# Kernel optimization log

Hardware: AMD Instinct MI355X
Metric: run time of the kernel (lower is better)

Reference implementation:

```python
import jax, jax.numpy as jnp
import numpy as np

DIM, NUM_HEADS, N_POINTS = 256, 8, 4
N_Q, N_KV = 32768, 32768


def setup_inputs() -> dict:
    key = jax.random.key(0)
    ks = jax.random.split(key, 16)
    C, H, P = DIM, NUM_HEADS, N_POINTS
    s = 1.0 / np.sqrt(C)
    inp = {
        "query": jax.random.normal(ks[0], (N_Q, C), jnp.float32),
        "key": jax.random.normal(ks[1], (N_KV, C), jnp.float32),
        "value": jax.random.normal(ks[2], (N_KV, C), jnp.float32),
        # reference_points: Linear(C, 2*H*P)
        "Wr": jax.random.normal(ks[3], (C, 2 * H * P), jnp.float32) * s,
        "br": jnp.zeros((2 * H * P,), jnp.float32),
        # offset_attn: Linear(C, H*P*2)
        "Wo": jax.random.normal(ks[4], (C, H * P * 2), jnp.float32) * s,
        "bo": jnp.zeros((H * P * 2,), jnp.float32),
        # value_proj: Linear(C, C)
        "Wv": jax.random.normal(ks[5], (C, C), jnp.float32) * s,
        "bv": jnp.zeros((C,), jnp.float32),
        # output_proj: Linear(C, C)
        "Wout": jax.random.normal(ks[6], (C, C), jnp.float32) * s,
        "bout": jnp.zeros((C,), jnp.float32),
    }
    return inp


def reference(query, key, value, Wr, br, Wo, bo, Wv, bv, Wout, bout):
    N, C = query.shape
    M = value.shape[0]
    H, P = NUM_HEADS, N_POINTS
    Ch = C // H

    # sampling locations in [0,1] (ref) plus unconstrained offsets
    ref = jax.nn.sigmoid((query @ Wr + br).reshape(N, H, P, 2))
    off = (query @ Wo + bo).reshape(N, H, P, 2)
    loc = ref + off                              # [N,H,P,2]

    # 1-D bilinear interpolation along the token axis. The original's
    # 4-term (wx,wy) expression algebraically collapses to a pure lerp in x:
    # (1-wx)(1-wy)+ (1-wx)wy = (1-wx), wx(1-wy)+wx*wy = wx.
    x = loc[..., 0] * (M - 1)                    # [N,H,P]
    x0 = jnp.clip(jnp.floor(x).astype(jnp.int32), 0, M - 1)
    x1 = jnp.clip(x0 + 1, 0, M - 1)
    wx = (x - x0.astype(x.dtype))[..., None]     # [N,H,P,1]

    hidx = jnp.arange(H)[None, :, None]          # head-aligned gather index

    def sample(table):                           # table: [M,H,Ch]
        g0 = table[x0, hidx]                     # [N,H,P,Ch]
        g1 = table[x1, hidx]
        return (1.0 - wx) * g0 + wx * g1

    v = (value @ Wv + bv).reshape(M, H, Ch)      # value_proj, split heads
    sv = sample(v)                               # [N,H,P,Ch] sampled values

    # attention weights from query/key: sample per-head keys at the same
    # locations, dot with per-head queries, softmax over the P points
    k = key.reshape(M, H, Ch)
    sk = sample(k)                               # [N,H,P,Ch]
    q = query.reshape(N, H, Ch)
    scores = jnp.einsum("nhc,nhpc->nhp", q, sk) / jnp.sqrt(
        jnp.asarray(Ch, query.dtype)
    )
    attn = jax.nn.softmax(scores, axis=-1)       # [N,H,P]

    out = jnp.einsum("nhp,nhpc->nhc", attn, sv).reshape(N, C)
    return out @ Wout + bout
```

## Files before the change

kernel.cpp:

```cpp
#include <hip/hip_runtime.h>
#include <hip/hip_bf16.h>
#include <stdint.h>

#define NQ    32768
#define NKV   32768
#define CDIM  256
#define NHEADS 8
#define NPTS  4

using bf16x8 = __attribute__((ext_vector_type(8))) short;
using f32x4  = __attribute__((ext_vector_type(4))) float;
using u16x8  = __attribute__((ext_vector_type(8))) ushort;

static __device__ __forceinline__ ushort f2bf(float f) {
  uint32_t u = __float_as_uint(f);
  return (ushort)((u + 0x7FFFu + ((u >> 16) & 1u)) >> 16);
}
static __device__ __forceinline__ float bf2f(ushort h) {
  return __uint_as_float(((uint32_t)h) << 16);
}
static __device__ __forceinline__ void async16(const void* g, void* l) {
  __builtin_amdgcn_global_load_lds(
      (const __attribute__((address_space(1))) uint32_t*)g,
      (__attribute__((address_space(3))) uint32_t*)l, 16, 0, 0);
}

__global__ __launch_bounds__(256) void transpose_w(const float* __restrict__ W,
                                                   ushort* __restrict__ WT) {
  int j = blockIdx.x, k = threadIdx.x;
  WT[j * 256 + k] = f2bf(W[k * 256 + j]);
}

__global__ __launch_bounds__(256) void gemm_mfma(
    const ushort* __restrict__ A, const ushort* __restrict__ BT,
    const float* __restrict__ bias, ushort* __restrict__ Cb,
    float* __restrict__ Cf, int out_bf16) {
  __shared__ ushort Alds[128 * 32];
  __shared__ ushort Blds[128 * 32];
  const int t = threadIdx.x;
  const int wave = t >> 6, lane = t & 63;
  const int mt = blockIdx.x >> 1, nt = blockIdx.x & 1;
  const int m0 = mt * 128, n0 = nt * 128;
  const int wr = wave >> 1, wc = wave & 1;
  const int r16 = lane & 15, kb = (lane >> 4) * 8;

  f32x4 acc[4][4] = {};

  for (int kt = 0; kt < 256; kt += 32) {
    __syncthreads();
#pragma unroll
    for (int it = 0; it < 2; ++it) {
      int c = it * 256 + t;
      int row = c >> 2, cc = c & 3;
      async16(A  + ((size_t)(m0 + row) * 256 + kt + cc * 8),
              Alds + (size_t)(it * 256 + wave * 64) * 8);
      async16(BT + ((size_t)(n0 + row) * 256 + kt + cc * 8),
              Blds + (size_t)(it * 256 + wave * 64) * 8);
    }
    __syncthreads();

    bf16x8 af[4], bfr[4];
#pragma unroll
    for (int m = 0; m < 4; ++m)
      af[m] = *(const bf16x8*)&Alds[(wr * 64 + m * 16 + r16) * 32 + kb];
#pragma unroll
    for (int n = 0; n < 4; ++n)
      bfr[n] = *(const bf16x8*)&Blds[(wc * 64 + n * 16 + r16) * 32 + kb];
#pragma unroll
    for (int m = 0; m < 4; ++m)
#pragma unroll
      for (int n = 0; n < 4; ++n)
        acc[m][n] = __builtin_amdgcn_mfma_f32_16x16x32_bf16(af[m], bfr[n],
                                                            acc[m][n], 0, 0, 0);
  }

  const int rg = lane >> 4;
#pragma unroll
  for (int m = 0; m < 4; ++m)
#pragma unroll
    for (int n = 0; n < 4; ++n) {
      int gc = n0 + wc * 64 + n * 16 + r16;
      float bb = bias[gc];
#pragma unroll
      for (int r = 0; r < 4; ++r) {
        int gr = m0 + wr * 64 + m * 16 + rg * 4 + r;
        float v = acc[m][n][r] + bb;
        if (out_bf16) Cb[(size_t)gr * 256 + gc] = f2bf(v);
        else          Cf[(size_t)gr * 256 + gc] = v;
      }
    }
}

__global__ __launch_bounds__(256) void gemm_mfma_fa(
    const float* __restrict__ Af, const ushort* __restrict__ BT,
    const float* __restrict__ bias, ushort* __restrict__ Cb) {
  __shared__ ushort Alds[128 * 32];
  __shared__ ushort Blds[128 * 32];
  const int t = threadIdx.x;
  const int wave = t >> 6, lane = t & 63;
  const int mt = blockIdx.x >> 1, nt = blockIdx.x & 1;
  const int m0 = mt * 128, n0 = nt * 128;
  const int wr = wave >> 1, wc = wave & 1;
  const int r16 = lane & 15, kb = (lane >> 4) * 8;

  f32x4 acc[4][4] = {};

  for (int kt = 0; kt < 256; kt += 32) {
    __syncthreads();
#pragma unroll
    for (int it = 0; it < 2; ++it) {
      int c = it * 256 + t;
      int row = c >> 2, cc = c & 3;
      async16(BT + ((size_t)(n0 + row) * 256 + kt + cc * 8),
              Blds + (size_t)(it * 256 + wave * 64) * 8);
    }
#pragma unroll
    for (int it = 0; it < 2; ++it) {
      int c = it * 256 + t;
      int row = c >> 2, cc = c & 3;
      const float* src = Af + (size_t)(m0 + row) * 256 + kt + cc * 8;
      f32x4 a = *(const f32x4*)src;
      f32x4 b = *(const f32x4*)(src + 4);
      u16x8 w;
#pragma unroll
      for (int e = 0; e < 4; ++e) { w[e] = f2bf(a[e]); w[4 + e] = f2bf(b[e]); }
      *(u16x8*)&Alds[(size_t)c * 8] = w;
    }
    __syncthreads();

    bf16x8 af[4], bfr[4];
#pragma unroll
    for (int m = 0; m < 4; ++m)
      af[m] = *(const bf16x8*)&Alds[(wr * 64 + m * 16 + r16) * 32 + kb];
#pragma unroll
    for (int n = 0; n < 4; ++n)
      bfr[n] = *(const bf16x8*)&Blds[(wc * 64 + n * 16 + r16) * 32 + kb];
#pragma unroll
    for (int m = 0; m < 4; ++m)
#pragma unroll
      for (int n = 0; n < 4; ++n)
        acc[m][n] = __builtin_amdgcn_mfma_f32_16x16x32_bf16(af[m], bfr[n],
                                                            acc[m][n], 0, 0, 0);
  }

  const int rg = lane >> 4;
#pragma unroll
  for (int m = 0; m < 4; ++m)
#pragma unroll
    for (int n = 0; n < 4; ++n) {
      int gc = n0 + wc * 64 + n * 16 + r16;
      float bb = bias[gc];
#pragma unroll
      for (int r = 0; r < 4; ++r) {
        int gr = m0 + wr * 64 + m * 16 + rg * 4 + r;
        Cb[(size_t)gr * 256 + gc] = f2bf(acc[m][n][r] + bb);
      }
    }
}

__global__ __launch_bounds__(256) void loc_gemm(const float* __restrict__ Q,
                                                const float* __restrict__ Wr,
                                                const float* __restrict__ Wo,
                                                float* __restrict__ locr) {
  __shared__ float AT[64][68];
  __shared__ float Bl[64][64];
  const int m0 = blockIdx.x * 64;
  const int t = threadIdx.x;
  const int tr = t >> 4, tc = t & 15;
  float acc[4][4] = {};

  for (int k0 = 0; k0 < 256; k0 += 64) {
    __syncthreads();
#pragma unroll
    for (int i = 0; i < 4; ++i) {
      int row = (t >> 4) + 16 * i;
      int kk = (t & 15) * 4;
      float4 v = *(const float4*)&Q[(size_t)(m0 + row) * 256 + k0 + kk];
      AT[kk + 0][row] = v.x; AT[kk + 1][row] = v.y;
      AT[kk + 2][row] = v.z; AT[kk + 3][row] = v.w;
    }
#pragma unroll
    for (int i = 0; i < 16; ++i) {
      int j = t & 63;
      int kk = (t >> 6) + 4 * i;
      float v = (j < 32) ? Wr[(size_t)(k0 + kk) * 64 + 2 * j]
                         : Wo[(size_t)(k0 + kk) * 64 + 2 * (j - 32)];
      Bl[kk][j] = v;
    }
    __syncthreads();
#pragma unroll 8
    for (int kk = 0; kk < 64; ++kk) {
      float4 a = *(const float4*)&AT[kk][tr * 4];
      float4 b = *(const float4*)&Bl[kk][tc * 4];
      float av[4] = {a.x, a.y, a.z, a.w};
      float bv4[4] = {b.x, b.y, b.z, b.w};
#pragma unroll
      for (int i = 0; i < 4; ++i)
#pragma unroll
        for (int jj = 0; jj < 4; ++jj) acc[i][jj] += av[i] * bv4[jj];
    }
  }
#pragma unroll
  for (int i = 0; i < 4; ++i)
#pragma unroll
    for (int jj = 0; jj < 4; ++jj)
      locr[(size_t)(m0 + tr * 4 + i) * 64 + tc * 4 + jj] = acc[i][jj];
}

__global__ __launch_bounds__(256, 2) void sample_attn(
    const float* __restrict__ query, const float* __restrict__ key,
    const ushort* __restrict__ vtab, const float* __restrict__ locr,
    const float* __restrict__ br, const float* __restrict__ bo,
    ushort* __restrict__ out2) {
  const int wave = threadIdx.x >> 6, lane = threadIdx.x & 63;
  const int half = lane >> 5;
  const int j = lane & 31;
  const int h = j >> 2, p = j & 3;
  const int n = blockIdx.x * 8 + wave * 2 + half;
  const int Mm1 = NKV - 1;

  float rr = locr[(size_t)n * 64 + j];
  float oo = locr[(size_t)n * 64 + 32 + j];
  float ref = 1.0f / (1.0f + expf(-(rr + br[2 * j])));
  float x = (ref + (oo + bo[2 * j])) * (float)Mm1;
  float xf = floorf(x);
  int x0 = (int)fminf(fmaxf(xf, 0.0f), (float)Mm1);
  int x1 = (x0 + 1 > Mm1) ? Mm1 : x0 + 1;
  float wx = x - (float)x0;
  float w0 = 1.0f - wx;

  const float*  kr0 = key  + (size_t)x0 * 256 + h * 32;
  const float*  kr1 = key  + (size_t)x1 * 256 + h * 32;
  const ushort* vr0 = vtab + (size_t)x0 * 256 + h * 32;
  const ushort* vr1 = vtab + (size_t)x1 * 256 + h * 32;
  const float*  qr  = query + (size_t)n * 256 + h * 32;

  f32x4 k0r[8], k1r[8], qv8[8];
  u16x8 v0r[4], v1r[4];
#pragma unroll
  for (int i = 0; i < 8; ++i) k0r[i] = *(const f32x4*)(kr0 + i * 4);
#pragma unroll
  for (int i = 0; i < 8; ++i) k1r[i] = *(const f32x4*)(kr1 + i * 4);
#pragma unroll
  for (int i = 0; i < 8; ++i) qv8[i] = *(const f32x4*)(qr + i * 4);
#pragma unroll
  for (int i = 0; i < 4; ++i) v0r[i] = *(const u16x8*)(vr0 + i * 8);
#pragma unroll
  for (int i = 0; i < 4; ++i) v1r[i] = *(const u16x8*)(vr1 + i * 8);
  __builtin_amdgcn_sched_barrier(0);

  float dot0 = 0.f, dot1 = 0.f;
#pragma unroll
  for (int i = 0; i < 8; ++i)
#pragma unroll
    for (int e = 0; e < 4; ++e) {
      dot0 += qv8[i][e] * k0r[i][e];
      dot1 += qv8[i][e] * k1r[i][e];
    }
  float score = (w0 * dot0 + wx * dot1) * 0.17677669529663687f;

  float m1 = fmaxf(score, __shfl_xor(score, 1, 64));
  float mx = fmaxf(m1, __shfl_xor(m1, 2, 64));
  float e = expf(score - mx);
  float s1 = e + __shfl_xor(e, 1, 64);
  float ssum = s1 + __shfl_xor(s1, 2, 64);
  float attn = e / ssum;

  float sv[32];
#pragma unroll
  for (int i = 0; i < 4; ++i)
#pragma unroll
    for (int ee = 0; ee < 8; ++ee)
      sv[i * 8 + ee] = w0 * bf2f((ushort)v0r[i][ee]) +
                       wx * bf2f((ushort)v1r[i][ee]);

  ushort ob[32];
#pragma unroll
  for (int c = 0; c < 32; ++c) {
    float t = attn * sv[c];
    t += __shfl_xor(t, 1, 64);
    t += __shfl_xor(t, 2, 64);
    ob[c] = f2bf(t);
  }
  if (p == 0) {
    ushort* dst = out2 + (size_t)n * 256 + h * 32;
#pragma unroll
    for (int c = 0; c < 32; c += 8) {
      u16x8 w;
#pragma unroll
      for (int ee = 0; ee < 8; ++ee) w[ee] = ob[c + ee];
      *(u16x8*)(dst + c) = w;
    }
  }
}

extern "C" void kernel_launch(void* const* d_in, const int* in_sizes, int n_in,
                              void* d_out, int out_size, void* d_ws, size_t ws_size,
                              hipStream_t stream) {
  const float* query = (const float*)d_in[0];
  const float* key   = (const float*)d_in[1];
  const float* value = (const float*)d_in[2];
  const float* Wr    = (const float*)d_in[3];
  const float* br    = (const float*)d_in[4];
  const float* Wo    = (const float*)d_in[5];
  const float* bo    = (const float*)d_in[6];
  const float* Wv    = (const float*)d_in[7];
  const float* bv    = (const float*)d_in[8];
  const float* Wout  = (const float*)d_in[9];
  const float* bout  = (const float*)d_in[10];
  float* out = (float*)d_out;

  char* ws = (char*)d_ws;
  ushort* out2  = (ushort*)(ws);
  ushort* vtab  = (ushort*)(ws + (16u << 20));
  float*  locr  = (float*) (ws + (32u << 20));
  ushort* WvT   = (ushort*)(ws + (40u << 20));
  ushort* WoT   = (ushort*)(ws + (40u << 20) + (1u << 17));

  transpose_w<<<256, 256, 0, stream>>>(Wv, WvT);
  transpose_w<<<256, 256, 0, stream>>>(Wout, WoT);
  gemm_mfma_fa<<<(NQ / 128) * 2, 256, 0, stream>>>(value, WvT, bv, vtab);
  loc_gemm<<<NQ / 64, 256, 0, stream>>>(query, Wr, Wo, locr);
  sample_attn<<<NQ / 8, 256, 0, stream>>>(query, key, vtab, locr, br, bo, out2);
  gemm_mfma<<<(NQ / 128) * 2, 256, 0, stream>>>(out2, WoT, bout, nullptr, out, 0);
}
```

Baseline: 108.2 us.

## Stage sampled key/value rows into LDS with async loads, one query per wave

The sampling kernel now gives each wave one query instead of two. Gathered key rows, value rows and the query row are copied into per-wave XOR-swizzled LDS buffers with global_load_lds, so the gathers are issued as fully coalesced 16-byte transfers. Lanes then read from LDS to compute the dot products and the weighted value sum. The output is written by all lanes with no p==0 masking, which removes the 32-step shuffle reduction, and staged vmcnt waits let the score and softmax math overlap the value loads. In exchange it uses about 52KB of LDS per block, which limits occupancy, and it launches twice as many blocks.

```diff
diff --git a/kernel.cpp b/kernel.cpp
--- a/kernel.cpp
+++ b/kernel.cpp
@@ -24,6 +24,8 @@
       (const __attribute__((address_space(1))) uint32_t*)g,
       (__attribute__((address_space(3))) uint32_t*)l, 16, 0, 0);
 }
+#define WAIT_VM(N) do { asm volatile("s_waitcnt vmcnt(" #N ")" ::: "memory"); \
+                        __builtin_amdgcn_sched_barrier(0); } while (0)
 
 __global__ __launch_bounds__(256) void transpose_w(const float* __restrict__ W,
                                                    ushort* __restrict__ WT) {
@@ -207,17 +209,19 @@
       locr[(size_t)(m0 + tr * 4 + i) * 64 + tc * 4 + jj] = acc[i][jj];
 }
 
-__global__ __launch_bounds__(256, 2) void sample_attn(
+__global__ __launch_bounds__(256) void sample_attn(
     const float* __restrict__ query, const float* __restrict__ key,
     const ushort* __restrict__ vtab, const float* __restrict__ locr,
     const float* __restrict__ br, const float* __restrict__ bo,
     ushort* __restrict__ out2) {
-  const int wave = threadIdx.x >> 6, lane = threadIdx.x & 63;
-  const int half = lane >> 5;
-  const int j = lane & 31;
-  const int h = j >> 2, p = j & 3;
-  const int n = blockIdx.x * 8 + wave * 2 + half;
+  __shared__ char smem[4][13312];
+  const int wave = threadIdx.x >> 6, l = threadIdx.x & 63;
+  const int j = l & 31;
+  const int n = blockIdx.x * 4 + wave;
   const int Mm1 = NKV - 1;
+  char* kbuf = smem[wave];
+  char* vbuf = kbuf + 8192;
+  char* qbuf = kbuf + 12288;
 
   float rr = locr[(size_t)n * 64 + j];
   float oo = locr[(size_t)n * 64 + 32 + j];
@@ -229,69 +233,86 @@
   float wx = x - (float)x0;
   float w0 = 1.0f - wx;
 
-  const float*  kr0 = key  + (size_t)x0 * 256 + h * 32;
-  const float*  kr1 = key  + (size_t)x1 * 256 + h * 32;
-  const ushort* vr0 = vtab + (size_t)x0 * 256 + h * 32;
-  const ushort* vr1 = vtab + (size_t)x1 * 256 + h * 32;
-  const float*  qr  = query + (size_t)n * 256 + h * 32;
-
-  f32x4 k0r[8], k1r[8], qv8[8];
-  u16x8 v0r[4], v1r[4];
-#pragma unroll
-  for (int i = 0; i < 8; ++i) k0r[i] = *(const f32x4*)(kr0 + i * 4);
-#pragma unroll
-  for (int i = 0; i < 8; ++i) k1r[i] = *(const f32x4*)(kr1 + i * 4);
-#pragma unroll
-  for (int i = 0; i < 8; ++i) qv8[i] = *(const f32x4*)(qr + i * 4);
-#pragma unroll
-  for (int i = 0; i < 4; ++i) v0r[i] = *(const u16x8*)(vr0 + i * 8);
-#pragma unroll
-  for (int i = 0; i < 4; ++i) v1r[i] = *(const u16x8*)(vr1 + i * 8);
-  __builtin_amdgcn_sched_barrier(0);
-
-  float dot0 = 0.f, dot1 = 0.f;
-#pragma unroll
-  for (int i = 0; i < 8; ++i)
-#pragma unroll
-    for (int e = 0; e < 4; ++e) {
-      dot0 += qv8[i][e] * k0r[i][e];
-      dot1 += qv8[i][e] * k1r[i][e];
-    }
-  float score = (w0 * dot0 + wx * dot1) * 0.17677669529663687f;
+  {
+    int hq = l >> 3, cq = l & 7;
+    async16(query + (size_t)n * 256 + hq * 32 + ((cq ^ hq) << 2), qbuf);
+  }
+  {
+    int ptg = l >> 3, s7 = l & 7;
+    int kch = s7 ^ ptg;
+#pragma unroll
+    for (int i = 0; i < 8; ++i) {
+      int pt = ((i & 3) << 3) + ptg;
+      int row = (i < 4) ? __shfl(x0, pt, 64) : __shfl(x1, pt, 64);
+      int hs = pt >> 2;
+      async16(key + (size_t)row * 256 + hs * 32 + (kch << 2), kbuf + i * 1024);
+    }
+  }
+  {
+    int cg = (l & 3) ^ ((l >> 2) & 3) ^ ((l >> 4) & 3);
+#pragma unroll
+    for (int i = 0; i < 4; ++i) {
+      int pt = ((i & 1) << 4) + (l >> 2);
+      int row = (i < 2) ? __shfl(x0, pt, 64) : __shfl(x1, pt, 64);
+      int hp = pt >> 2;
+      async16(vtab + (size_t)row * 256 + hp * 32 + cg * 8, vbuf + i * 1024);
+    }
+  }
+
+  WAIT_VM(4);
+
+  float dot = 0.f;
+  {
+    int h = (l & 31) >> 2;
+#pragma unroll
+    for (int c = 0; c < 8; ++c) {
+      f32x4 qc = *(const f32x4*)(qbuf + ((h << 3) + (c ^ h)) * 16);
+      f32x4 kc = *(const f32x4*)(kbuf + l * 128 + ((c ^ (l & 7)) << 4));
+#pragma unroll
+      for (int e = 0; e < 4; ++e) dot += qc[e] * kc[e];
+    }
+  }
+  float other = __shfl_xor(dot, 32, 64);
+  float d0 = (l < 32) ? dot : other;
+  float d1 = (l < 32) ? other : dot;
+  float score = (w0 * d0 + wx * d1) * 0.17677669529663687f;
 
   float m1 = fmaxf(score, __shfl_xor(score, 1, 64));
   float mx = fmaxf(m1, __shfl_xor(m1, 2, 64));
-  float e = expf(score - mx);
-  float s1 = e + __shfl_xor(e, 1, 64);
+  float e0 = expf(score - mx);
+  float s1 = e0 + __shfl_xor(e0, 1, 64);
   float ssum = s1 + __shfl_xor(s1, 2, 64);
-  float attn = e / ssum;
-
-  float sv[32];
-#pragma unroll
-  for (int i = 0; i < 4; ++i)
-#pragma unroll
-    for (int ee = 0; ee < 8; ++ee)
-      sv[i * 8 + ee] = w0 * bf2f((ushort)v0r[i][ee]) +
-                       wx * bf2f((ushort)v1r[i][ee]);
-
-  ushort ob[32];
-#pragma unroll
-  for (int c = 0; c < 32; ++c) {
-    float t = attn * sv[c];
-    t += __shfl_xor(t, 1, 64);
-    t += __shfl_xor(t, 2, 64);
-    ob[c] = f2bf(t);
-  }
-  if (p == 0) {
-    ushort* dst = out2 + (size_t)n * 256 + h * 32;
-#pragma unroll
-    for (int c = 0; c < 32; c += 8) {
-      u16x8 w;
-#pragma unroll
-      for (int ee = 0; ee < 8; ++ee) w[ee] = ob[c + ee];
-      *(u16x8*)(dst + c) = w;
-    }
-  }
+  float attn = e0 / ssum;
+  float c0 = attn * w0, c1 = attn * wx;
+
+  const int oh = l >> 3, os = l & 7;
+  float cc0[4], cc1[4];
+#pragma unroll
+  for (int m = 0; m < 4; ++m) {
+    cc0[m] = __shfl(c0, oh * 4 + m, 64);
+    cc1[m] = __shfl(c1, oh * 4 + m, 64);
+  }
+
+  WAIT_VM(0);
+
+  float acc[4] = {};
+#pragma unroll
+  for (int m = 0; m < 4; ++m) {
+    int pt = oh * 4 + m;
+    int slot = (os >> 1) ^ m ^ (oh & 3);
+    int off = slot * 16 + (os & 1) * 8;
+    ushort4 v0 = *(const ushort4*)(vbuf + pt * 64 + off);
+    ushort4 v1 = *(const ushort4*)(vbuf + (pt + 32) * 64 + off);
+#pragma unroll
+    for (int e = 0; e < 4; ++e) {
+      float ve0 = bf2f((&v0.x)[e]), ve1 = bf2f((&v1.x)[e]);
+      acc[e] += cc0[m] * ve0 + cc1[m] * ve1;
+    }
+  }
+  ushort4 ow;
+#pragma unroll
+  for (int e = 0; e < 4; ++e) (&ow.x)[e] = f2bf(acc[e]);
+  *(ushort4*)(out2 + (size_t)n * 256 + oh * 32 + os * 4) = ow;
 }
 
 extern "C" void kernel_launch(void* const* d_in, const int* in_sizes, int n_in,
@@ -321,6 +342,6 @@
   transpose_w<<<256, 256, 0, stream>>>(Wout, WoT);
   gemm_mfma_fa<<<(NQ / 128) * 2, 256, 0, stream>>>(value, WvT, bv, vtab);
   loc_gemm<<<NQ / 64, 256, 0, stream>>>(query, Wr, Wo, locr);
-  sample_attn<<<NQ / 8, 256, 0, stream>>>(query, key, vtab, locr, br, bo, out2);
+  sample_attn<<<NQ / 4, 256, 0, stream>>>(query, key, vtab, locr, br, bo, out2);
   gemm_mfma<<<(NQ / 128) * 2, 256, 0, stream>>>(out2, WoT, bout, nullptr, out, 0);
 }
```

New measurement: 102.3 us. -5.4%, faster.
